# Optimization experiments

Hardware: AMD Instinct MI355X
Metric: run time of the kernel (lower is better)

Reference implementation:

```python
import jax, jax.numpy as jnp
import numpy as np

N_NODES = 50000
N_EDGES = 800000
IN_DIM, HID_DIM, OUT_DIM = 128, 256, 64


def setup_inputs() -> dict:
    key = jax.random.key(0)
    k1, k2, k3, k4 = jax.random.split(key, 4)
    x = jax.random.normal(k1, (N_NODES, IN_DIM), dtype=jnp.float32)
    edge_index = jax.random.randint(k2, (2, N_EDGES), 0, N_NODES, dtype=jnp.int32)
    # Glorot-ish scaled weights
    W1 = jax.random.normal(k3, (IN_DIM, HID_DIM), dtype=jnp.float32) * (1.0 / np.sqrt(IN_DIM))
    W2 = jax.random.normal(k4, (HID_DIM, OUT_DIM), dtype=jnp.float32) * (1.0 / np.sqrt(HID_DIM))
    b1 = jnp.zeros((HID_DIM,), dtype=jnp.float32)
    b2 = jnp.zeros((OUT_DIM,), dtype=jnp.float32)
    return {"x": x, "edge_index": edge_index, "W1": W1, "b1": b1, "W2": W2, "b2": b2}


def _gcn_conv(x, src, dst, deg_inv_sqrt, W, b):
    # transform first (PyG GCNConv order), then edge-normalized scatter-add
    h = x @ W                                        # [N, D_out]
    norm = deg_inv_sqrt[src] * deg_inv_sqrt[dst]     # [E]
    msgs = h[src] * norm[:, None]                    # [E, D_out]
    agg = jax.ops.segment_sum(msgs, dst, num_segments=x.shape[0])
    return agg + b


def reference(x, edge_index, W1, b1, W2, b2):
    n = x.shape[0]
    loops = jnp.arange(n, dtype=edge_index.dtype)
    src = jnp.concatenate([edge_index[0], loops])    # add self-loops
    dst = jnp.concatenate([edge_index[1], loops])
    deg = jax.ops.segment_sum(jnp.ones_like(dst, dtype=x.dtype), dst, num_segments=n)
    deg_inv_sqrt = jnp.where(deg > 0, jax.lax.rsqrt(jnp.maximum(deg, 1e-12)), 0.0)
    h = jax.nn.relu(_gcn_conv(x, src, dst, deg_inv_sqrt, W1, b1))
    h = _gcn_conv(h, src, dst, deg_inv_sqrt, W2, b2)
    return jax.nn.log_softmax(h, axis=1)
```

## Files before the change

kernel.cpp:

```cpp
#include <hip/hip_runtime.h>
#include <hip/hip_bf16.h>
#include <math.h>

#define N_NODES 50000
#define N_EDGES 800000
#define IN_DIM 128
#define HID_DIM 256
#define OUT_DIM 64
#define NPART 196
#define CAP 8192
#define CHUNK 2048
#define NPB ((N_EDGES + CHUNK - 1) / CHUNK)

typedef __attribute__((ext_vector_type(8))) short bf16x8;
typedef __attribute__((ext_vector_type(4))) short short4v;
typedef __attribute__((ext_vector_type(4))) float f32x4;

__device__ inline short f2bf(float f) {
    unsigned u = __float_as_uint(f);
    unsigned r = (u + 0x7fffu + ((u >> 16) & 1u)) >> 16;
    return (short)r;
}
__device__ inline float bf_lo(unsigned u) { return __uint_as_float(u << 16); }
__device__ inline float bf_hi(unsigned u) { return __uint_as_float(u & 0xffff0000u); }

__global__ __launch_bounds__(256) void part1_pack_kernel(const int* __restrict__ src,
                                                         const int* __restrict__ dst,
                                                         int* __restrict__ coarseCursor,
                                                         uint2* __restrict__ sedge,
                                                         const float* __restrict__ W1,
                                                         const float* __restrict__ W2,
                                                         short* __restrict__ Bp1,
                                                         short* __restrict__ Bp2, int E) {
    __shared__ int cnt_l[NPART];
    __shared__ int pref[NPART];
    __shared__ int gbase[NPART];
    __shared__ int ws4[4];
    __shared__ uint2 stage[CHUNK];
    int tid = threadIdx.x;
    if (blockIdx.x >= NPB) {
        int idx = (blockIdx.x - NPB) * 256 + tid;
        const float* W; short* Bp; int N;
        const int T1 = (IN_DIM / 32) * (HID_DIM / 16) * 64;
        const int T2 = (HID_DIM / 32) * (OUT_DIM / 16) * 64;
        if (idx < T1) { W = W1; Bp = Bp1; N = HID_DIM; }
        else { idx -= T1; if (idx >= T2) return; W = W2; Bp = Bp2; N = OUT_DIM; }
        int lane = idx & 63;
        int frag = idx >> 6;
        int ntiles = N >> 4;
        int nt = frag % ntiles;
        int kt = frag / ntiles;
        int col = nt * 16 + (lane & 15);
        int krow = kt * 32 + (lane >> 4) * 8;
        bf16x8 pk;
        #pragma unroll
        for (int j = 0; j < 8; j++) pk[j] = f2bf(W[(size_t)(krow + j) * N + col]);
        *((bf16x8*)(Bp + (size_t)idx * 8)) = pk;
        return;
    }
    int e0 = blockIdx.x * CHUNK;
    if (tid < NPART) cnt_l[tid] = 0;
    __syncthreads();
    int es[CHUNK / 256], ed[CHUNK / 256];
    #pragma unroll
    for (int j = 0; j < CHUNK / 256; j++) {
        int e = e0 + j * 256 + tid;
        if (e < E) {
            es[j] = src[e]; ed[j] = dst[e];
            atomicAdd(&cnt_l[ed[j] >> 8], 1);
        } else ed[j] = -1;
    }
    __syncthreads();
    int lane = tid & 63, wid = tid >> 6;
    int v = (tid < NPART) ? cnt_l[tid] : 0;
    int s = v;
    #pragma unroll
    for (int off = 1; off < 64; off <<= 1) {
        int t = __shfl_up(s, off, 64);
        if (lane >= off) s += t;
    }
    if (lane == 63) ws4[wid] = s;
    __syncthreads();
    int wp = 0;
    #pragma unroll
    for (int w = 0; w < 4; w++) wp += (w < wid) ? ws4[w] : 0;
    int excl = s - v + wp;
    if (tid < NPART) pref[tid] = excl;
    __syncthreads();
    if (tid < NPART) cnt_l[tid] = excl;
    __syncthreads();
    #pragma unroll
    for (int j = 0; j < CHUNK / 256; j++) {
        if (ed[j] >= 0) {
            int c = ed[j] >> 8;
            int p = atomicAdd(&cnt_l[c], 1);
            stage[p] = make_uint2((unsigned)es[j], (unsigned)ed[j]);
        }
    }
    __syncthreads();
    if (tid < NPART) {
        int cl = cnt_l[tid] - pref[tid];
        gbase[tid] = (cl > 0) ? (tid * CAP + atomicAdd(&coarseCursor[tid], cl)) : 0;
    }
    __syncthreads();
    int total = (e0 + CHUNK <= E) ? CHUNK : (E - e0);
    for (int i = tid; i < total; i += 256) {
        uint2 ev = stage[i];
        int c = (int)(ev.y >> 8);
        sedge[gbase[c] + (i - pref[c])] = ev;
    }
}

__global__ __launch_bounds__(256) void part2_kernel(const uint2* __restrict__ sedge,
                                                    const int* __restrict__ coarseCnt,
                                                    int* __restrict__ offs,
                                                    int* __restrict__ cntg,
                                                    float* __restrict__ dis,
                                                    int* __restrict__ ssrc,
                                                    const float* __restrict__ x,
                                                    short* __restrict__ xb, int n) {
    __shared__ int kcnt[256];
    __shared__ int ws4[4];
    __shared__ float sdis[256];
    int b = blockIdx.x, tid = threadIdx.x;
    int base = b * CAP;
    int cb = coarseCnt[b];
    kcnt[tid] = 0;
    __syncthreads();
    for (int i = tid; i < cb; i += 256) {
        uint2 ev = sedge[base + i];
        atomicAdd(&kcnt[ev.y & 255], 1);
    }
    __syncthreads();
    int v = kcnt[tid];
    int lane = tid & 63, wid = tid >> 6;
    int s = v;
    #pragma unroll
    for (int off = 1; off < 64; off <<= 1) {
        int t = __shfl_up(s, off, 64);
        if (lane >= off) s += t;
    }
    if (lane == 63) ws4[wid] = s;
    __syncthreads();
    int wp = 0;
    #pragma unroll
    for (int w = 0; w < 4; w++) wp += (w < wid) ? ws4[w] : 0;
    int excl = s - v + wp;
    int node = b * 256 + tid;
    float dn = rsqrtf((float)v + 1.0f);
    if (node < n) {
        offs[node] = base + excl;
        cntg[node] = v;
        dis[node] = dn;
    }
    sdis[tid] = dn;
    __syncthreads();
    kcnt[tid] = base + excl;
    __syncthreads();
    for (int i = tid; i < cb; i += 256) {
        uint2 ev = sedge[base + i];
        int pos = atomicAdd(&kcnt[ev.y & 255], 1);
        ssrc[pos] = (int)ev.x;
    }
    int rlane = tid & 31, rgrp = tid >> 5;
    for (int rb = 0; rb < 32; rb++) {
        int row = rb * 8 + rgrp;
        int nd = b * 256 + row;
        if (nd >= n) break;
        float d2 = sdis[row];
        float4 vv = ((const float4*)(x + (size_t)nd * IN_DIM))[rlane];
        short4v o = {f2bf(vv.x * d2), f2bf(vv.y * d2), f2bf(vv.z * d2), f2bf(vv.w * d2)};
        *((short4v*)(xb + (size_t)nd * IN_DIM + rlane * 4)) = o;
    }
}

__global__ void agg1_kernel(const short* __restrict__ xb, const int* __restrict__ ssrc,
                            const int* __restrict__ offs, const int* __restrict__ cnt,
                            const float* __restrict__ dis, short* __restrict__ aggx, int n) {
    int lane = threadIdx.x & 63;
    int node = blockIdx.x * (blockDim.x >> 6) + (threadIdx.x >> 6);
    if (node >= n) return;
    int grp = lane >> 4, l16 = lane & 15;
    int start = offs[node], c = cnt[node];
    float acc[8] = {};
    int j = grp;
    for (; j + 12 < c; j += 16) {
        int s0 = ssrc[start + j];
        int s1 = ssrc[start + j + 4];
        int s2 = ssrc[start + j + 8];
        int s3 = ssrc[start + j + 12];
        uint4 p0 = *((const uint4*)(xb + (size_t)s0 * IN_DIM + l16 * 8));
        uint4 p1 = *((const uint4*)(xb + (size_t)s1 * IN_DIM + l16 * 8));
        uint4 p2 = *((const uint4*)(xb + (size_t)s2 * IN_DIM + l16 * 8));
        uint4 p3 = *((const uint4*)(xb + (size_t)s3 * IN_DIM + l16 * 8));
        acc[0] += bf_lo(p0.x); acc[1] += bf_hi(p0.x); acc[2] += bf_lo(p0.y); acc[3] += bf_hi(p0.y);
        acc[4] += bf_lo(p0.z); acc[5] += bf_hi(p0.z); acc[6] += bf_lo(p0.w); acc[7] += bf_hi(p0.w);
        acc[0] += bf_lo(p1.x); acc[1] += bf_hi(p1.x); acc[2] += bf_lo(p1.y); acc[3] += bf_hi(p1.y);
        acc[4] += bf_lo(p1.z); acc[5] += bf_hi(p1.z); acc[6] += bf_lo(p1.w); acc[7] += bf_hi(p1.w);
        acc[0] += bf_lo(p2.x); acc[1] += bf_hi(p2.x); acc[2] += bf_lo(p2.y); acc[3] += bf_hi(p2.y);
        acc[4] += bf_lo(p2.z); acc[5] += bf_hi(p2.z); acc[6] += bf_lo(p2.w); acc[7] += bf_hi(p2.w);
        acc[0] += bf_lo(p3.x); acc[1] += bf_hi(p3.x); acc[2] += bf_lo(p3.y); acc[3] += bf_hi(p3.y);
        acc[4] += bf_lo(p3.z); acc[5] += bf_hi(p3.z); acc[6] += bf_lo(p3.w); acc[7] += bf_hi(p3.w);
    }
    for (; j < c; j += 4) {
        int s0 = ssrc[start + j];
        uint4 p0 = *((const uint4*)(xb + (size_t)s0 * IN_DIM + l16 * 8));
        acc[0] += bf_lo(p0.x); acc[1] += bf_hi(p0.x); acc[2] += bf_lo(p0.y); acc[3] += bf_hi(p0.y);
        acc[4] += bf_lo(p0.z); acc[5] += bf_hi(p0.z); acc[6] += bf_lo(p0.w); acc[7] += bf_hi(p0.w);
    }
    #pragma unroll
    for (int k = 0; k < 8; k++) {
        acc[k] += __shfl_xor(acc[k], 16, 64);
        acc[k] += __shfl_xor(acc[k], 32, 64);
    }
    if (grp == 0) {
        float dn = dis[node];
        uint4 pk = *((const uint4*)(xb + (size_t)node * IN_DIM + l16 * 8));
        acc[0] += bf_lo(pk.x); acc[1] += bf_hi(pk.x); acc[2] += bf_lo(pk.y); acc[3] += bf_hi(pk.y);
        acc[4] += bf_lo(pk.z); acc[5] += bf_hi(pk.z); acc[6] += bf_lo(pk.w); acc[7] += bf_hi(pk.w);
        bf16x8 o;
        #pragma unroll
        for (int k = 0; k < 8; k++) o[k] = f2bf(acc[k] * dn);
        *((bf16x8*)(aggx + (size_t)node * IN_DIM + l16 * 8)) = o;
    }
}

#define H1_STRIDE 264
__global__ __launch_bounds__(256) void gemm_fused_kernel(const short* __restrict__ A,
                                                         const short* __restrict__ Bp1,
                                                         const short* __restrict__ Bp2,
                                                         const float* __restrict__ b1,
                                                         const float* __restrict__ dis,
                                                         short* __restrict__ h2, int M) {
    __shared__ short lds_h1[4][16][H1_STRIDE];
    int lane = threadIdx.x & 63;
    int w = threadIdx.x >> 6;
    int rowBase = blockIdx.x * 64 + w * 16;
    int arow = rowBase + (lane & 15);
    int kseg = lane >> 4;
    int col0 = lane & 15;

    constexpr int NT1 = HID_DIM / 16;
    f32x4 acc1[NT1] = {};
    #pragma unroll
    for (int kt = 0; kt < IN_DIM / 32; kt++) {
        bf16x8 a = {};
        if (arow < M)
            a = *((const bf16x8*)(A + (size_t)arow * IN_DIM + kt * 32 + kseg * 8));
        #pragma unroll
        for (int nt = 0; nt < NT1; nt++) {
            bf16x8 b = *((const bf16x8*)(Bp1 + ((size_t)(kt * NT1 + nt) * 64 + lane) * 8));
            acc1[nt] = __builtin_amdgcn_mfma_f32_16x16x32_bf16(a, b, acc1[nt], 0, 0, 0);
        }
    }
    #pragma unroll
    for (int nt = 0; nt < NT1; nt++) {
        float bv = b1[nt * 16 + col0];
        #pragma unroll
        for (int i = 0; i < 4; i++) {
            float v = fmaxf(acc1[nt][i] + bv, 0.0f);
            lds_h1[w][kseg * 4 + i][nt * 16 + col0] = f2bf(v);
        }
    }
    constexpr int NT2 = OUT_DIM / 16;
    f32x4 acc2[NT2] = {};
    #pragma unroll
    for (int kt = 0; kt < HID_DIM / 32; kt++) {
        bf16x8 a = *((const bf16x8*)&lds_h1[w][lane & 15][kt * 32 + kseg * 8]);
        #pragma unroll
        for (int nt = 0; nt < NT2; nt++) {
            bf16x8 b = *((const bf16x8*)(Bp2 + ((size_t)(kt * NT2 + nt) * 64 + lane) * 8));
            acc2[nt] = __builtin_amdgcn_mfma_f32_16x16x32_bf16(a, b, acc2[nt], 0, 0, 0);
        }
    }
    #pragma unroll
    for (int i = 0; i < 4; i++) {
        int r = rowBase + kseg * 4 + i;
        if (r >= M) continue;
        float sc = dis[r];
        #pragma unroll
        for (int nt = 0; nt < NT2; nt++)
            h2[(size_t)r * OUT_DIM + nt * 16 + col0] = f2bf(acc2[nt][i] * sc);
    }
}

__global__ void agg2_kernel(const short* __restrict__ h2, const int* __restrict__ ssrc,
                            const int* __restrict__ offs, const int* __restrict__ cnt,
                            const float* __restrict__ dis, const float* __restrict__ b2,
                            float* __restrict__ out, int n) {
    int lane = threadIdx.x & 63;
    int node = blockIdx.x * (blockDim.x >> 6) + (threadIdx.x >> 6);
    if (node >= n) return;
    int grp = lane >> 4, l16 = lane & 15;
    int start = offs[node], c = cnt[node];
    float acc[4] = {};
    int j = grp;
    for (; j + 12 < c; j += 16) {
        int s0 = ssrc[start + j];
        int s1 = ssrc[start + j + 4];
        int s2 = ssrc[start + j + 8];
        int s3 = ssrc[start + j + 12];
        uint2 p0 = *((const uint2*)(h2 + (size_t)s0 * OUT_DIM + l16 * 4));
        uint2 p1 = *((const uint2*)(h2 + (size_t)s1 * OUT_DIM + l16 * 4));
        uint2 p2 = *((const uint2*)(h2 + (size_t)s2 * OUT_DIM + l16 * 4));
        uint2 p3 = *((const uint2*)(h2 + (size_t)s3 * OUT_DIM + l16 * 4));
        acc[0] += bf_lo(p0.x); acc[1] += bf_hi(p0.x); acc[2] += bf_lo(p0.y); acc[3] += bf_hi(p0.y);
        acc[0] += bf_lo(p1.x); acc[1] += bf_hi(p1.x); acc[2] += bf_lo(p1.y); acc[3] += bf_hi(p1.y);
        acc[0] += bf_lo(p2.x); acc[1] += bf_hi(p2.x); acc[2] += bf_lo(p2.y); acc[3] += bf_hi(p2.y);
        acc[0] += bf_lo(p3.x); acc[1] += bf_hi(p3.x); acc[2] += bf_lo(p3.y); acc[3] += bf_hi(p3.y);
    }
    for (; j < c; j += 4) {
        int s0 = ssrc[start + j];
        uint2 p0 = *((const uint2*)(h2 + (size_t)s0 * OUT_DIM + l16 * 4));
        acc[0] += bf_lo(p0.x); acc[1] += bf_hi(p0.x); acc[2] += bf_lo(p0.y); acc[3] += bf_hi(p0.y);
    }
    #pragma unroll
    for (int k = 0; k < 4; k++) {
        acc[k] += __shfl_xor(acc[k], 16, 64);
        acc[k] += __shfl_xor(acc[k], 32, 64);
    }
    float dn = dis[node];
    uint2 pv = *((const uint2*)(h2 + (size_t)node * OUT_DIM + l16 * 4));
    float4 bb = ((const float4*)b2)[l16];
    acc[0] = (acc[0] + bf_lo(pv.x)) * dn + bb.x;
    acc[1] = (acc[1] + bf_hi(pv.x)) * dn + bb.y;
    acc[2] = (acc[2] + bf_lo(pv.y)) * dn + bb.z;
    acc[3] = (acc[3] + bf_hi(pv.y)) * dn + bb.w;
    float m = fmaxf(fmaxf(acc[0], acc[1]), fmaxf(acc[2], acc[3]));
    #pragma unroll
    for (int off = 1; off < 16; off <<= 1) m = fmaxf(m, __shfl_xor(m, off, 64));
    float ex = expf(acc[0] - m) + expf(acc[1] - m) + expf(acc[2] - m) + expf(acc[3] - m);
    #pragma unroll
    for (int off = 1; off < 16; off <<= 1) ex += __shfl_xor(ex, off, 64);
    float ls = m + logf(ex);
    if (grp == 0) {
        float4 o = {acc[0] - ls, acc[1] - ls, acc[2] - ls, acc[3] - ls};
        ((float4*)(out + (size_t)node * OUT_DIM))[l16] = o;
    }
}

extern "C" void kernel_launch(void* const* d_in, const int* in_sizes, int n_in,
                              void* d_out, int out_size, void* d_ws, size_t ws_size,
                              hipStream_t stream) {
    const float* x  = (const float*)d_in[0];
    const int*   ei = (const int*)d_in[1];
    const float* W1 = (const float*)d_in[2];
    const float* b1 = (const float*)d_in[3];
    const float* W2 = (const float*)d_in[4];
    const float* b2 = (const float*)d_in[5];
    float* out = (float*)d_out;
    char* ws = (char*)d_ws;

    const int* srcp = ei;
    const int* dstp = ei + N_EDGES;

    int*   coarseCursor = (int*)(ws);
    int*   offs   = (int*)(ws + 4096);
    int*   cntg   = (int*)(ws + 262144);
    float* dis    = (float*)(ws + 524288);
    short* Bp1    = (short*)(ws + 786432);
    short* Bp2    = (short*)(ws + 851968);
    int*   ssrc   = (int*)(ws + 917504);
    uint2* sedge  = (uint2*)(ws + 7340032);
    short* aggx   = (short*)(ws + 7340032);
    short* xb     = (short*)(ws + 20185088);
    short* h2     = (short*)(ws + 32985088);

    hipMemsetAsync(coarseCursor, 0, NPART * 4, stream);

    part1_pack_kernel<<<NPB + 24, 256, 0, stream>>>(srcp, dstp, coarseCursor, sedge,
                                                    W1, W2, Bp1, Bp2, N_EDGES);
    part2_kernel<<<NPART, 256, 0, stream>>>(sedge, coarseCursor, offs, cntg, dis, ssrc,
                                            x, xb, N_NODES);
    agg1_kernel<<<(N_NODES + 3) / 4, 256, 0, stream>>>(xb, ssrc, offs, cntg, dis, aggx, N_NODES);
    gemm_fused_kernel<<<(N_NODES + 63) / 64, 256, 0, stream>>>(aggx, Bp1, Bp2, b1, dis,
                                                               h2, N_NODES);
    agg2_kernel<<<(N_NODES + 3) / 4, 256, 0, stream>>>(h2, ssrc, offs, cntg, dis, b2, out, N_NODES);
}
```

Before: 206.2 us.

## Widen per-lane feature slices and preload neighbor indices via wave shuffles in aggregation

Both aggregation kernels now split each wavefront into 8 groups of 8 lanes instead of 4 groups of 16, so each lane handles twice as many features with wider loads. The first 64 neighbor indices are loaded once, coalesced, into a register per lane and broadcast with __shfl, which removes the serial dependent index loads. Each round gathers 16 neighbors, with zero-weight masking for the padded slots. This raises gather-level parallelism and cuts index-load latency, at the cost of more registers, wasted masked loads for low-degree nodes, and an extra shuffle reduction stage. Blocks are hard-coded to 4 wavefronts.

```diff
diff --git a/kernel.cpp b/kernel.cpp
--- a/kernel.cpp
+++ b/kernel.cpp
@@ -178,50 +178,73 @@
                             const int* __restrict__ offs, const int* __restrict__ cnt,
                             const float* __restrict__ dis, short* __restrict__ aggx, int n) {
     int lane = threadIdx.x & 63;
-    int node = blockIdx.x * (blockDim.x >> 6) + (threadIdx.x >> 6);
+    int node = blockIdx.x * 4 + (threadIdx.x >> 6);
     if (node >= n) return;
-    int grp = lane >> 4, l16 = lane & 15;
+    int grp = lane >> 3, l8 = lane & 7;
     int start = offs[node], c = cnt[node];
-    float acc[8] = {};
-    int j = grp;
-    for (; j + 12 < c; j += 16) {
+    int vidx = (lane < c) ? ssrc[start + lane] : 0;
+    float acc[16] = {};
+    int lim = (c < 64) ? c : 64;
+    int rounds = (lim + 15) >> 4;
+    for (int r = 0; r < rounds; r++) {
+        int j0 = r * 16 + grp;
+        int j1 = j0 + 8;
+        int i0 = (j0 < 63) ? j0 : 63;
+        int i1 = (j1 < 63) ? j1 : 63;
+        int s0 = __shfl(vidx, i0, 64);
+        int s1 = __shfl(vidx, i1, 64);
+        float g0 = (j0 < lim) ? 1.0f : 0.0f;
+        float g1 = (j1 < lim) ? 1.0f : 0.0f;
+        const uint4* r0 = (const uint4*)(xb + (size_t)s0 * IN_DIM + l8 * 16);
+        const uint4* r1 = (const uint4*)(xb + (size_t)s1 * IN_DIM + l8 * 16);
+        uint4 a0 = r0[0], a1 = r0[1];
+        uint4 b0 = r1[0], b1 = r1[1];
+        acc[0]  += g0 * bf_lo(a0.x); acc[1]  += g0 * bf_hi(a0.x);
+        acc[2]  += g0 * bf_lo(a0.y); acc[3]  += g0 * bf_hi(a0.y);
+        acc[4]  += g0 * bf_lo(a0.z); acc[5]  += g0 * bf_hi(a0.z);
+        acc[6]  += g0 * bf_lo(a0.w); acc[7]  += g0 * bf_hi(a0.w);
+        acc[8]  += g0 * bf_lo(a1.x); acc[9]  += g0 * bf_hi(a1.x);
+        acc[10] += g0 * bf_lo(a1.y); acc[11] += g0 * bf_hi(a1.y);
+        acc[12] += g0 * bf_lo(a1.z); acc[13] += g0 * bf_hi(a1.z);
+        acc[14] += g0 * bf_lo(a1.w); acc[15] += g0 * bf_hi(a1.w);
+        acc[0]  += g1 * bf_lo(b0.x); acc[1]  += g1 * bf_hi(b0.x);
+        acc[2]  += g1 * bf_lo(b0.y); acc[3]  += g1 * bf_hi(b0.y);
+        acc[4]  += g1 * bf_lo(b0.z); acc[5]  += g1 * bf_hi(b0.z);
+        acc[6]  += g1 * bf_lo(b0.w); acc[7]  += g1 * bf_hi(b0.w);
+        acc[8]  += g1 * bf_lo(b1.x); acc[9]  += g1 * bf_hi(b1.x);
+        acc[10] += g1 * bf_lo(b1.y); acc[11] += g1 * bf_hi(b1.y);
+        acc[12] += g1 * bf_lo(b1.z); acc[13] += g1 * bf_hi(b1.z);
+        acc[14] += g1 * bf_lo(b1.w); acc[15] += g1 * bf_hi(b1.w);
+    }
+    for (int j = 64 + grp; j < c; j += 8) {
         int s0 = ssrc[start + j];
-        int s1 = ssrc[start + j + 4];
-        int s2 = ssrc[start + j + 8];
-        int s3 = ssrc[start + j + 12];
-        uint4 p0 = *((const uint4*)(xb + (size_t)s0 * IN_DIM + l16 * 8));
-        uint4 p1 = *((const uint4*)(xb + (size_t)s1 * IN_DIM + l16 * 8));
-        uint4 p2 = *((const uint4*)(xb + (size_t)s2 * IN_DIM + l16 * 8));
-        uint4 p3 = *((const uint4*)(xb + (size_t)s3 * IN_DIM + l16 * 8));
-        acc[0] += bf_lo(p0.x); acc[1] += bf_hi(p0.x); acc[2] += bf_lo(p0.y); acc[3] += bf_hi(p0.y);
-        acc[4] += bf_lo(p0.z); acc[5] += bf_hi(p0.z); acc[6] += bf_lo(p0.w); acc[7] += bf_hi(p0.w);
-        acc[0] += bf_lo(p1.x); acc[1] += bf_hi(p1.x); acc[2] += bf_lo(p1.y); acc[3] += bf_hi(p1.y);
-        acc[4] += bf_lo(p1.z); acc[5] += bf_hi(p1.z); acc[6] += bf_lo(p1.w); acc[7] += bf_hi(p1.w);
-        acc[0] += bf_lo(p2.x); acc[1] += bf_hi(p2.x); acc[2] += bf_lo(p2.y); acc[3] += bf_hi(p2.y);
-        acc[4] += bf_lo(p2.z); acc[5] += bf_hi(p2.z); acc[6] += bf_lo(p2.w); acc[7] += bf_hi(p2.w);
-        acc[0] += bf_lo(p3.x); acc[1] += bf_hi(p3.x); acc[2] += bf_lo(p3.y); acc[3] += bf_hi(p3.y);
-        acc[4] += bf_lo(p3.z); acc[5] += bf_hi(p3.z); acc[6] += bf_lo(p3.w); acc[7] += bf_hi(p3.w);
-    }
-    for (; j < c; j += 4) {
-        int s0 = ssrc[start + j];
-        uint4 p0 = *((const uint4*)(xb + (size_t)s0 * IN_DIM + l16 * 8));
-        acc[0] += bf_lo(p0.x); acc[1] += bf_hi(p0.x); acc[2] += bf_lo(p0.y); acc[3] += bf_hi(p0.y);
-        acc[4] += bf_lo(p0.z); acc[5] += bf_hi(p0.z); acc[6] += bf_lo(p0.w); acc[7] += bf_hi(p0.w);
-    }
-    #pragma unroll
-    for (int k = 0; k < 8; k++) {
+        const uint4* r0 = (const uint4*)(xb + (size_t)s0 * IN_DIM + l8 * 16);
+        uint4 a0 = r0[0], a1 = r0[1];
+        acc[0]  += bf_lo(a0.x); acc[1]  += bf_hi(a0.x); acc[2]  += bf_lo(a0.y); acc[3]  += bf_hi(a0.y);
+        acc[4]  += bf_lo(a0.z); acc[5]  += bf_hi(a0.z); acc[6]  += bf_lo(a0.w); acc[7]  += bf_hi(a0.w);
+        acc[8]  += bf_lo(a1.x); acc[9]  += bf_hi(a1.x); acc[10] += bf_lo(a1.y); acc[11] += bf_hi(a1.y);
+        acc[12] += bf_lo(a1.z); acc[13] += bf_hi(a1.z); acc[14] += bf_lo(a1.w); acc[15] += bf_hi(a1.w);
+    }
+    #pragma unroll
+    for (int k = 0; k < 16; k++) {
+        acc[k] += __shfl_xor(acc[k], 8, 64);
         acc[k] += __shfl_xor(acc[k], 16, 64);
         acc[k] += __shfl_xor(acc[k], 32, 64);
     }
     if (grp == 0) {
         float dn = dis[node];
-        uint4 pk = *((const uint4*)(xb + (size_t)node * IN_DIM + l16 * 8));
-        acc[0] += bf_lo(pk.x); acc[1] += bf_hi(pk.x); acc[2] += bf_lo(pk.y); acc[3] += bf_hi(pk.y);
-        acc[4] += bf_lo(pk.z); acc[5] += bf_hi(pk.z); acc[6] += bf_lo(pk.w); acc[7] += bf_hi(pk.w);
-        bf16x8 o;
-        #pragma unroll
-        for (int k = 0; k < 8; k++) o[k] = f2bf(acc[k] * dn);
-        *((bf16x8*)(aggx + (size_t)node * IN_DIM + l16 * 8)) = o;
+        const uint4* rs = (const uint4*)(xb + (size_t)node * IN_DIM + l8 * 16);
+        uint4 a0 = rs[0], a1 = rs[1];
+        acc[0]  += bf_lo(a0.x); acc[1]  += bf_hi(a0.x); acc[2]  += bf_lo(a0.y); acc[3]  += bf_hi(a0.y);
+        acc[4]  += bf_lo(a0.z); acc[5]  += bf_hi(a0.z); acc[6]  += bf_lo(a0.w); acc[7]  += bf_hi(a0.w);
+        acc[8]  += bf_lo(a1.x); acc[9]  += bf_hi(a1.x); acc[10] += bf_lo(a1.y); acc[11] += bf_hi(a1.y);
+        acc[12] += bf_lo(a1.z); acc[13] += bf_hi(a1.z); acc[14] += bf_lo(a1.w); acc[15] += bf_hi(a1.w);
+        bf16x8 o0, o1;
+        #pragma unroll
+        for (int k = 0; k < 8; k++) { o0[k] = f2bf(acc[k] * dn); o1[k] = f2bf(acc[k + 8] * dn); }
+        short* dst0 = aggx + (size_t)node * IN_DIM + l8 * 16;
+        *((bf16x8*)dst0) = o0;
+        *((bf16x8*)(dst0 + 8)) = o1;
     }
 }
 
@@ -289,53 +312,74 @@
                             const float* __restrict__ dis, const float* __restrict__ b2,
                             float* __restrict__ out, int n) {
     int lane = threadIdx.x & 63;
-    int node = blockIdx.x * (blockDim.x >> 6) + (threadIdx.x >> 6);
+    int node = blockIdx.x * 4 + (threadIdx.x >> 6);
     if (node >= n) return;
-    int grp = lane >> 4, l16 = lane & 15;
+    int grp = lane >> 3, l8 = lane & 7;
     int start = offs[node], c = cnt[node];
-    float acc[4] = {};
-    int j = grp;
-    for (; j + 12 < c; j += 16) {
+    int vidx = (lane < c) ? ssrc[start + lane] : 0;
+    float acc[8] = {};
+    int lim = (c < 64) ? c : 64;
+    int rounds = (lim + 15) >> 4;
+    for (int r = 0; r < rounds; r++) {
+        int j0 = r * 16 + grp;
+        int j1 = j0 + 8;
+        int i0 = (j0 < 63) ? j0 : 63;
+        int i1 = (j1 < 63) ? j1 : 63;
+        int s0 = __shfl(vidx, i0, 64);
+        int s1 = __shfl(vidx, i1, 64);
+        float g0 = (j0 < lim) ? 1.0f : 0.0f;
+        float g1 = (j1 < lim) ? 1.0f : 0.0f;
+        uint4 p0 = *((const uint4*)(h2 + (size_t)s0 * OUT_DIM + l8 * 8));
+        uint4 p1 = *((const uint4*)(h2 + (size_t)s1 * OUT_DIM + l8 * 8));
+        acc[0] += g0 * bf_lo(p0.x); acc[1] += g0 * bf_hi(p0.x);
+        acc[2] += g0 * bf_lo(p0.y); acc[3] += g0 * bf_hi(p0.y);
+        acc[4] += g0 * bf_lo(p0.z); acc[5] += g0 * bf_hi(p0.z);
+        acc[6] += g0 * bf_lo(p0.w); acc[7] += g0 * bf_hi(p0.w);
+        acc[0] += g1 * bf_lo(p1.x); acc[1] += g1 * bf_hi(p1.x);
+        acc[2] += g1 * bf_lo(p1.y); acc[3] += g1 * bf_hi(p1.y);
+        acc[4] += g1 * bf_lo(p1.z); acc[5] += g1 * bf_hi(p1.z);
+        acc[6] += g1 * bf_lo(p1.w); acc[7] += g1 * bf_hi(p1.w);
+    }
+    for (int j = 64 + grp; j < c; j += 8) {
         int s0 = ssrc[start + j];
-        int s1 = ssrc[start + j + 4];
-        int s2 = ssrc[start + j + 8];
-        int s3 = ssrc[start + j + 12];
-        uint2 p0 = *((const uint2*)(h2 + (size_t)s0 * OUT_DIM + l16 * 4));
-        uint2 p1 = *((const uint2*)(h2 + (size_t)s1 * OUT_DIM + l16 * 4));
-        uint2 p2 = *((const uint2*)(h2 + (size_t)s2 * OUT_DIM + l16 * 4));
-        uint2 p3 = *((const uint2*)(h2 + (size_t)s3 * OUT_DIM + l16 * 4));
+        uint4 p0 = *((const uint4*)(h2 + (size_t)s0 * OUT_DIM + l8 * 8));
         acc[0] += bf_lo(p0.x); acc[1] += bf_hi(p0.x); acc[2] += bf_lo(p0.y); acc[3] += bf_hi(p0.y);
-        acc[0] += bf_lo(p1.x); acc[1] += bf_hi(p1.x); acc[2] += bf_lo(p1.y); acc[3] += bf_hi(p1.y);
-        acc[0] += bf_lo(p2.x); acc[1] += bf_hi(p2.x); acc[2] += bf_lo(p2.y); acc[3] += bf_hi(p2.y);
-        acc[0] += bf_lo(p3.x); acc[1] += bf_hi(p3.x); acc[2] += bf_lo(p3.y); acc[3] += bf_hi(p3.y);
-    }
-    for (; j < c; j += 4) {
-        int s0 = ssrc[start + j];
-        uint2 p0 = *((const uint2*)(h2 + (size_t)s0 * OUT_DIM + l16 * 4));
-        acc[0] += bf_lo(p0.x); acc[1] += bf_hi(p0.x); acc[2] += bf_lo(p0.y); acc[3] += bf_hi(p0.y);
-    }
-    #pragma unroll
-    for (int k = 0; k < 4; k++) {
+        acc[4] += bf_lo(p0.z); acc[5] += bf_hi(p0.z); acc[6] += bf_lo(p0.w); acc[7] += bf_hi(p0.w);
+    }
+    #pragma unroll
+    for (int k = 0; k < 8; k++) {
+        acc[k] += __shfl_xor(acc[k], 8, 64);
         acc[k] += __shfl_xor(acc[k], 16, 64);
         acc[k] += __shfl_xor(acc[k], 32, 64);
     }
     float dn = dis[node];
-    uint2 pv = *((const uint2*)(h2 + (size_t)node * OUT_DIM + l16 * 4));
-    float4 bb = ((const float4*)b2)[l16];
-    acc[0] = (acc[0] + bf_lo(pv.x)) * dn + bb.x;
-    acc[1] = (acc[1] + bf_hi(pv.x)) * dn + bb.y;
-    acc[2] = (acc[2] + bf_lo(pv.y)) * dn + bb.z;
-    acc[3] = (acc[3] + bf_hi(pv.y)) * dn + bb.w;
-    float m = fmaxf(fmaxf(acc[0], acc[1]), fmaxf(acc[2], acc[3]));
-    #pragma unroll
-    for (int off = 1; off < 16; off <<= 1) m = fmaxf(m, __shfl_xor(m, off, 64));
-    float ex = expf(acc[0] - m) + expf(acc[1] - m) + expf(acc[2] - m) + expf(acc[3] - m);
-    #pragma unroll
-    for (int off = 1; off < 16; off <<= 1) ex += __shfl_xor(ex, off, 64);
+    uint4 pv = *((const uint4*)(h2 + (size_t)node * OUT_DIM + l8 * 8));
+    float4 bb0 = ((const float4*)b2)[l8 * 2];
+    float4 bb1 = ((const float4*)b2)[l8 * 2 + 1];
+    acc[0] = (acc[0] + bf_lo(pv.x)) * dn + bb0.x;
+    acc[1] = (acc[1] + bf_hi(pv.x)) * dn + bb0.y;
+    acc[2] = (acc[2] + bf_lo(pv.y)) * dn + bb0.z;
+    acc[3] = (acc[3] + bf_hi(pv.y)) * dn + bb0.w;
+    acc[4] = (acc[4] + bf_lo(pv.z)) * dn + bb1.x;
+    acc[5] = (acc[5] + bf_hi(pv.z)) * dn + bb1.y;
+    acc[6] = (acc[6] + bf_lo(pv.w)) * dn + bb1.z;
+    acc[7] = (acc[7] + bf_hi(pv.w)) * dn + bb1.w;
+    float m = acc[0];
+    #pragma unroll
+    for (int k = 1; k < 8; k++) m = fmaxf(m, acc[k]);
+    #pragma unroll
+    for (int off = 1; off < 8; off <<= 1) m = fmaxf(m, __shfl_xor(m, off, 64));
+    float ex = 0.0f;
+    #pragma unroll
+    for (int k = 0; k < 8; k++) ex += expf(acc[k] - m);
+    #pragma unroll
+    for (int off = 1; off < 8; off <<= 1) ex += __shfl_xor(ex, off, 64);
     float ls = m + logf(ex);
     if (grp == 0) {
-        float4 o = {acc[0] - ls, acc[1] - ls, acc[2] - ls, acc[3] - ls};
-        ((float4*)(out + (size_t)node * OUT_DIM))[l16] = o;
+        float4 o0 = {acc[0] - ls, acc[1] - ls, acc[2] - ls, acc[3] - ls};
+        float4 o1 = {acc[4] - ls, acc[5] - ls, acc[6] - ls, acc[7] - ls};
+        ((float4*)(out + (size_t)node * OUT_DIM))[l8 * 2] = o0;
+        ((float4*)(out + (size_t)node * OUT_DIM))[l8 * 2 + 1] = o1;
     }
 }
 
```

Result: no change. 203.0 us, median of 2 (-1.5%).
